# Performance work log

Hardware: AMD Instinct MI355X
Metric: run time of the kernel (lower is better)

## Reference

```python
import jax, jax.numpy as jnp
import numpy as np

THRESH = 0.1

def _ternary_ste(w):
    # STE: forward = ternary(w), backward = identity
    wq = jnp.where(w > THRESH, 1.0, jnp.where(w < -THRESH, -1.0, 0.0))
    return w + jax.lax.stop_gradient(wq - w)

def _act_quant_ste(x):
    # training-mode ActivationQuantizer: scale = 127/max|x| (buffer update, detached)
    scale = jax.lax.stop_gradient(127.0 / jnp.max(jnp.abs(x)))
    xq = jnp.clip(jnp.round(x * scale), -128.0, 127.0) / scale
    return x + jax.lax.stop_gradient(xq - x)

def setup_inputs() -> dict:
    key = jax.random.key(0)
    k1, k2, k3, k4, k5 = jax.random.split(key, 5)
    B, D_IN, D_H, D_OUT = 8192, 784, 4096, 10
    x = jax.random.normal(k1, (B, D_IN), dtype=jnp.float32)
    w1 = jax.random.normal(k2, (D_H, D_IN), dtype=jnp.float32) * 0.05
    b1 = jax.random.normal(k3, (D_H,), dtype=jnp.float32) * 0.01
    w2 = jax.random.normal(k4, (D_OUT, D_H), dtype=jnp.float32) * 0.05
    b2 = jax.random.normal(k5, (D_OUT,), dtype=jnp.float32) * 0.01
    return {"x": x, "w1": w1, "b1": b1, "w2": w2, "b2": b2}

def reference(x, w1, b1, w2, b2):
    x = x.reshape(-1, 784)
    h = x @ _ternary_ste(w1).T + b1          # [B, D_H]
    h = jax.nn.relu(h)
    h = _act_quant_ste(h)
    logits = h @ _ternary_ste(w2).T + b2     # [B, D_OUT]
    return jax.nn.log_softmax(logits, axis=1)
```

## Files before the change

kernel.cpp:

```cpp
#include <hip/hip_runtime.h>

#define M_B   8192
#define K_IN  784
#define KPAD  832
#define N_H   4096
#define N_OUT 10
#define BM    128
#define BN    128
#define BK    64

typedef __attribute__((ext_vector_type(8))) short bf16x8;
typedef __attribute__((ext_vector_type(4))) float f32x4;
typedef unsigned short u16;
typedef unsigned int   u32;

__device__ __forceinline__ u16 f2bf(float f) {
    union { float f; u32 u; } v; v.f = f;
    u32 r = (v.u + 0x7fffu + ((v.u >> 16) & 1u)) >> 16;
    return (u16)r;
}
__device__ __forceinline__ void load_lds16(const void* g, void* l) {
    __builtin_amdgcn_global_load_lds(
        (const __attribute__((address_space(1))) void*)g,
        (__attribute__((address_space(3))) void*)l, 16, 0, 0);
}

__global__ void prep_all(const float* __restrict__ x, const float* __restrict__ w1,
                         const float* __restrict__ w2,
                         u16* __restrict__ xb, u16* __restrict__ w1b,
                         signed char* __restrict__ w2c, float* __restrict__ plog) {
    const int blk = blockIdx.x;
    const int tid = threadIdx.x;
    if (blk < 3328) {
        int idx = blk * 256 + tid;
        int row = idx / 104;
        int col = (idx - row * 104) * 8;
        u16 v[8];
        if (col < K_IN) {
            const float4* p = (const float4*)(x + (size_t)row * K_IN + col);
            float4 a = p[0], b = p[1];
            v[0] = f2bf(a.x); v[1] = f2bf(a.y); v[2] = f2bf(a.z); v[3] = f2bf(a.w);
            v[4] = f2bf(b.x); v[5] = f2bf(b.y); v[6] = f2bf(b.z); v[7] = f2bf(b.w);
        } else {
            #pragma unroll
            for (int i = 0; i < 8; ++i) v[i] = 0;
        }
        *(uint4*)(xb + (size_t)row * KPAD + col) = *(const uint4*)v;
    } else if (blk < 4992) {
        int idx = (blk - 3328) * 256 + tid;
        int row = idx / 104;
        int col = (idx - row * 104) * 8;
        u16 v[8];
        if (col < K_IN) {
            const float4* p = (const float4*)(w1 + (size_t)row * K_IN + col);
            float4 a = p[0], b = p[1];
            float ff[8] = {a.x, a.y, a.z, a.w, b.x, b.y, b.z, b.w};
            #pragma unroll
            for (int i = 0; i < 8; ++i)
                v[i] = ff[i] > 0.1f ? 0x3F80u : (ff[i] < -0.1f ? 0xBF80u : 0u);
        } else {
            #pragma unroll
            for (int i = 0; i < 8; ++i) v[i] = 0;
        }
        *(uint4*)(w1b + (size_t)row * KPAD + col) = *(const uint4*)v;
    } else if (blk < 5008) {
        int k = (blk - 4992) * 256 + tid;
        if (k >= N_H) return;
        signed char v[16];
        #pragma unroll
        for (int o = 0; o < 16; ++o) v[o] = 0;
        #pragma unroll
        for (int o = 0; o < N_OUT; ++o) {
            float f = w2[(size_t)o * N_H + k];
            v[o] = f > 0.1f ? 1 : (f < -0.1f ? -1 : 0);
        }
        *(int4*)(w2c + (size_t)k * 16) = *(const int4*)v;
    } else {
        int idx = (blk - 5008) * 256 + tid;
        ((uint4*)plog)[idx] = make_uint4(0, 0, 0, 0);
    }
}

__global__ __launch_bounds__(256, 3) void gemm_fused(
    const u16* __restrict__ Wb,
    const u16* __restrict__ Xb,
    const float* __restrict__ b1,
    const signed char* __restrict__ W2c,
    float* __restrict__ plog)
{
    __shared__ __align__(16) u16 As[BM * BK];
    __shared__ __align__(16) u16 Bs[BN * BK];
    __shared__ __align__(16) signed char sW2[128 * 16];
    __shared__ float sB1[128];

    const int tid  = threadIdx.x;
    const int lane = tid & 63;
    const int wave = tid >> 6;
    const int wr = wave >> 1, wc = wave & 1;
    const int bm = blockIdx.x;
    const int bn = blockIdx.y;

    if (tid < 128) {
        *(int4*)&sW2[tid * 16] = *(const int4*)(W2c + (size_t)(bm * 128 + tid) * 16);
        sB1[tid] = b1[bm * 128 + tid];
    }

    f32x4 acc[4][4] = {};

    const u16* ga[4]; u16* la[4];
    #pragma unroll
    for (int j = 0; j < 4; ++j) {
        int s = tid + 256 * j;
        int grow = s >> 3;
        int gcol = (((s & 7) ^ ((s >> 3) & 7)) << 3);
        ga[j] = Wb + (size_t)(bm * BM + grow) * KPAD + gcol;
        la[j] = &As[s * 8];
    }
    const u16* gb[4]; u16* lb[4];
    #pragma unroll
    for (int j = 0; j < 4; ++j) {
        int s = tid + 256 * j;
        int grow = s >> 3;
        int gcol = (((s & 7) ^ ((s >> 3) & 7)) << 3);
        gb[j] = Xb + (size_t)(bn * BN + grow) * KPAD + gcol;
        lb[j] = &Bs[s * 8];
    }

    const int rA = (wr * 64 + (lane & 15)) * BK;
    const int rB = (wc * 64 + (lane & 15)) * BK;
    const int c0 = (((lane >> 4) ^ (lane & 7)) << 3);

    for (int t = 0; t < 13; ++t) {
        #pragma unroll
        for (int j = 0; j < 4; ++j) { load_lds16(ga[j], la[j]); ga[j] += BK; }
        #pragma unroll
        for (int j = 0; j < 4; ++j) { load_lds16(gb[j], lb[j]); gb[j] += BK; }
        __syncthreads();

        #pragma unroll
        for (int h = 0; h < 2; ++h) {
            const int ch = c0 ^ (h << 5);
            bf16x8 af[4], bfr[4];
            #pragma unroll
            for (int i = 0; i < 4; ++i) af[i]  = *(const bf16x8*)&As[rA + i * 16 * BK + ch];
            #pragma unroll
            for (int j = 0; j < 4; ++j) bfr[j] = *(const bf16x8*)&Bs[rB + j * 16 * BK + ch];
            #pragma unroll
            for (int i = 0; i < 4; ++i)
                #pragma unroll
                for (int j = 0; j < 4; ++j)
                    acc[i][j] = __builtin_amdgcn_mfma_f32_16x16x32_bf16(
                        af[i], bfr[j], acc[i][j], 0, 0, 0);
        }
        __syncthreads();
    }

    const int quad = lane >> 4;
    const int o = lane & 15;

    bf16x8 wf[4];
    #pragma unroll
    for (int i = 0; i < 4; ++i) {
        #pragma unroll
        for (int jj = 0; jj < 4; ++jj) {
            signed char s8 = sW2[(wr * 64 + i * 16 + quad * 4 + jj) * 16 + o];
            wf[i][jj] = (s8 == 0) ? (short)0 : (s8 > 0 ? (short)0x3F80 : (short)0xBF80);
            wf[i][jj + 4] = 0;
        }
    }
    float4 bias[4];
    #pragma unroll
    for (int i = 0; i < 4; ++i)
        bias[i] = *(const float4*)&sB1[wr * 64 + i * 16 + quad * 4];

    f32x4 d2[4] = {};
    #pragma unroll
    for (int jb = 0; jb < 4; ++jb) {
        #pragma unroll
        for (int i = 0; i < 4; ++i) {
            bf16x8 hf;
            const float* bi = (const float*)&bias[i];
            #pragma unroll
            for (int r = 0; r < 4; ++r) {
                float v = fmaxf(acc[i][jb][r] + bi[r], 0.f);
                hf[r] = (short)f2bf(v);
                hf[r + 4] = 0;
            }
            d2[jb] = __builtin_amdgcn_mfma_f32_16x16x32_bf16(hf, wf[i], d2[jb], 0, 0, 0);
        }
    }

    if (o < N_OUT) {
        #pragma unroll
        for (int jb = 0; jb < 4; ++jb) {
            const int bbase = bn * BN + wc * 64 + jb * 16 + quad * 4;
            #pragma unroll
            for (int r = 0; r < 4; ++r)
                atomicAdd(&plog[(size_t)(bbase + r) * 16 + o], d2[jb][r]);
        }
    }
}

__global__ __launch_bounds__(128) void lsm_out(
    const float* __restrict__ plog,
    const float* __restrict__ b2,
    float* __restrict__ out)
{
    const int b = blockIdx.x * 128 + threadIdx.x;

    float4 p0 = *(const float4*)(plog + (size_t)b * 16);
    float4 p1 = *(const float4*)(plog + (size_t)b * 16 + 4);
    float4 p2 = *(const float4*)(plog + (size_t)b * 16 + 8);
    float p[10] = {p0.x, p0.y, p0.z, p0.w, p1.x, p1.y, p1.z, p1.w, p2.x, p2.y};

    float lg[N_OUT], mx = -1e30f;
    #pragma unroll
    for (int o = 0; o < N_OUT; ++o) {
        lg[o] = p[o] + b2[o];
        mx = fmaxf(mx, lg[o]);
    }
    float se = 0.f;
    #pragma unroll
    for (int o = 0; o < N_OUT; ++o) se += expf(lg[o] - mx);
    const float lse = logf(se) + mx;
    float* op = out + (size_t)b * N_OUT;
    #pragma unroll
    for (int o = 0; o < N_OUT; ++o) op[o] = lg[o] - lse;
}

extern "C" void kernel_launch(void* const* d_in, const int* in_sizes, int n_in,
                              void* d_out, int out_size, void* d_ws, size_t ws_size,
                              hipStream_t stream) {
    const float* x  = (const float*)d_in[0];
    const float* w1 = (const float*)d_in[1];
    const float* b1 = (const float*)d_in[2];
    const float* w2 = (const float*)d_in[3];
    const float* b2 = (const float*)d_in[4];
    float* out = (float*)d_out;

    char* ws = (char*)d_ws;
    u16* xb  = (u16*)(ws);
    u16* w1b = (u16*)(ws + 13631488);
    signed char* w2c = (signed char*)(ws + 20447232);
    float* plog = (float*)(ws + 20512768);

    prep_all<<<5136, 256, 0, stream>>>(x, w1, w2, xb, w1b, w2c, plog);
    gemm_fused<<<dim3(32, 64), 256, 0, stream>>>(w1b, xb, b1, w2c, plog);
    lsm_out<<<64, 128, 0, stream>>>(plog, b2, out);
}
```

Before: 144.2 us.

## Rewrite fused GEMM as 256x256 tile with double-buffered LDS pipeline

Replaces the 128x128 single-buffered GEMM tile with a 256x256 tile computed by 8 waves, using a 128 KB double-buffered LDS layout. Global-to-LDS loads for later k-tiles are issued while MFMAs run on the current buffer, with manual vmcnt/lgkmcnt waits, barriers, sched_barrier and setprio. It also remaps block indices for L2 locality and reads W2/b1 directly from global memory in the epilogue. The larger tile cuts redundant global loads, but it raises register pressure (128 accumulator floats per thread), limits occupancy, and adds many barriers.

```diff
diff --git a/kernel.cpp b/kernel.cpp
--- a/kernel.cpp
+++ b/kernel.cpp
@@ -5,9 +5,7 @@
 #define KPAD  832
 #define N_H   4096
 #define N_OUT 10
-#define BM    128
-#define BN    128
-#define BK    64
+#define TILES 13
 
 typedef __attribute__((ext_vector_type(8))) short bf16x8;
 typedef __attribute__((ext_vector_type(4))) float f32x4;
@@ -81,119 +79,156 @@
     }
 }
 
-__global__ __launch_bounds__(256, 3) void gemm_fused(
+
+#define BAR()    asm volatile("s_barrier" ::: "memory")
+#define LGKM0()  asm volatile("s_waitcnt lgkmcnt(0)" ::: "memory")
+#define VM6()    asm volatile("s_waitcnt vmcnt(6)" ::: "memory")
+#define VM0()    asm volatile("s_waitcnt vmcnt(0)" ::: "memory")
+#define SCHED0() __builtin_amdgcn_sched_barrier(0)
+
+__global__ __launch_bounds__(512, 2) void gemm_fused(
     const u16* __restrict__ Wb,
     const u16* __restrict__ Xb,
     const float* __restrict__ b1,
     const signed char* __restrict__ W2c,
     float* __restrict__ plog)
 {
-    __shared__ __align__(16) u16 As[BM * BK];
-    __shared__ __align__(16) u16 Bs[BN * BK];
-    __shared__ __align__(16) signed char sW2[128 * 16];
-    __shared__ float sB1[128];
+    __shared__ __align__(128) u16 lds[65536];
 
     const int tid  = threadIdx.x;
     const int lane = tid & 63;
     const int wave = tid >> 6;
-    const int wr = wave >> 1, wc = wave & 1;
-    const int bm = blockIdx.x;
-    const int bn = blockIdx.y;
-
-    if (tid < 128) {
-        *(int4*)&sW2[tid * 16] = *(const int4*)(W2c + (size_t)(bm * 128 + tid) * 16);
-        sB1[tid] = b1[bm * 128 + tid];
-    }
-
-    f32x4 acc[4][4] = {};
-
-    const u16* ga[4]; u16* la[4];
-    #pragma unroll
-    for (int j = 0; j < 4; ++j) {
-        int s = tid + 256 * j;
-        int grow = s >> 3;
-        int gcol = (((s & 7) ^ ((s >> 3) & 7)) << 3);
-        ga[j] = Wb + (size_t)(bm * BM + grow) * KPAD + gcol;
-        la[j] = &As[s * 8];
-    }
-    const u16* gb[4]; u16* lb[4];
-    #pragma unroll
-    for (int j = 0; j < 4; ++j) {
-        int s = tid + 256 * j;
-        int grow = s >> 3;
-        int gcol = (((s & 7) ^ ((s >> 3) & 7)) << 3);
-        gb[j] = Xb + (size_t)(bn * BN + grow) * KPAD + gcol;
-        lb[j] = &Bs[s * 8];
-    }
-
-    const int rA = (wr * 64 + (lane & 15)) * BK;
-    const int rB = (wc * 64 + (lane & 15)) * BK;
-    const int c0 = (((lane >> 4) ^ (lane & 7)) << 3);
-
-    for (int t = 0; t < 13; ++t) {
-        #pragma unroll
-        for (int j = 0; j < 4; ++j) { load_lds16(ga[j], la[j]); ga[j] += BK; }
-        #pragma unroll
-        for (int j = 0; j < 4; ++j) { load_lds16(gb[j], lb[j]); gb[j] += BK; }
-        __syncthreads();
-
-        #pragma unroll
-        for (int h = 0; h < 2; ++h) {
-            const int ch = c0 ^ (h << 5);
-            bf16x8 af[4], bfr[4];
-            #pragma unroll
-            for (int i = 0; i < 4; ++i) af[i]  = *(const bf16x8*)&As[rA + i * 16 * BK + ch];
-            #pragma unroll
-            for (int j = 0; j < 4; ++j) bfr[j] = *(const bf16x8*)&Bs[rB + j * 16 * BK + ch];
-            #pragma unroll
-            for (int i = 0; i < 4; ++i)
-                #pragma unroll
-                for (int j = 0; j < 4; ++j)
-                    acc[i][j] = __builtin_amdgcn_mfma_f32_16x16x32_bf16(
-                        af[i], bfr[j], acc[i][j], 0, 0, 0);
-        }
-        __syncthreads();
-    }
+    const int wr = wave >> 2;
+    const int wc = wave & 3;
+
+    const int bid = blockIdx.x;
+    const int swz = (bid & 7) * 64 + (bid >> 3);
+    const int bm = swz & 15;
+    const int bn = swz >> 4;
+
+    const int srow = tid >> 2;
+    const int co   = (tid & 3) ^ ((srow >> 1) & 3);
+    const u16* gA0 = Wb + (size_t)(bm * 256 + srow) * KPAD + co * 8;
+    const u16* gA1 = gA0 + (size_t)128 * KPAD;
+    const u16* gB0 = Xb + (size_t)(bn * 256 + srow) * KPAD + co * 8;
+    const u16* gB1 = gB0 + (size_t)128 * KPAD;
+
+    const int lm    = lane & 15;
+    const int aLane = lm * 32 + ((((lane >> 4) ^ (lm >> 1)) & 3) << 3);
+    const int aBase = wr * 4096 + aLane;
+    const int bBase = 32768 + wc * 2048 + aLane;
+
+    f32x4 acc[8][4] = {};
+    bf16x8 bfr[4];
+
+#define STAGE(SOP, SP0, SP1, ST, SKH)                                      \
+    if ((ST) < TILES) {                                                    \
+      const int rb = (SOP)*32768 + ((ST)&1)*16384 + (SKH)*8192 + tid*8;    \
+      load_lds16(SP0 + (ST)*64 + (SKH)*32, lds + rb);                      \
+      load_lds16(SP1 + (ST)*64 + (SKH)*32, lds + rb + 4096);               \
+    }
+
+#define RD_A(BUF, KH, IH)                                                  \
+    { const u16* pa = lds + aBase + ((BUF)*16384 + (KH)*8192 + (IH)*2048); \
+      af[0] = *(const bf16x8*)(pa);                                        \
+      af[1] = *(const bf16x8*)(pa + 512);                                  \
+      af[2] = *(const bf16x8*)(pa + 1024);                                 \
+      af[3] = *(const bf16x8*)(pa + 1536); }
+
+#define RD_B(BUF, KH)                                                      \
+    { const u16* pb = lds + bBase + ((BUF)*16384 + (KH)*8192);             \
+      bfr[0] = *(const bf16x8*)(pb);                                       \
+      bfr[1] = *(const bf16x8*)(pb + 512);                                 \
+      bfr[2] = *(const bf16x8*)(pb + 1024);                                \
+      bfr[3] = *(const bf16x8*)(pb + 1536); }
+
+#define MFMA16(IH)                                                         \
+    __builtin_amdgcn_s_setprio(1);                                         \
+    _Pragma("unroll")                                                      \
+    for (int ii = 0; ii < 4; ++ii)                                         \
+      _Pragma("unroll")                                                    \
+      for (int jb = 0; jb < 4; ++jb)                                       \
+        acc[(IH)*4 + ii][jb] = __builtin_amdgcn_mfma_f32_16x16x32_bf16(    \
+            af[ii], bfr[jb], acc[(IH)*4 + ii][jb], 0, 0, 0);               \
+    __builtin_amdgcn_s_setprio(0);
+
+    STAGE(0, gA0, gA1, 0, 0);
+    STAGE(1, gB0, gB1, 0, 0);
+    STAGE(0, gA0, gA1, 0, 1);
+    STAGE(1, gB0, gB1, 0, 1);
+    STAGE(1, gB0, gB1, 1, 0);
+    STAGE(0, gA0, gA1, 1, 0);
+    STAGE(1, gB0, gB1, 1, 1);
+    VM6(); BAR();
+
+    #pragma unroll 1
+    for (int i = 0; i < 6; ++i) {
+        const int t1 = 2 * i + 1, t2 = 2 * i + 2, t3 = 2 * i + 3;
+        { bf16x8 af[4]; RD_A(0,0,0); RD_B(0,0); STAGE(0, gA0, gA1, t1, 1);
+          BAR(); LGKM0(); SCHED0(); MFMA16(0); } BAR();
+        { bf16x8 af[4]; RD_A(0,0,1);            STAGE(1, gB0, gB1, t2, 0);
+          BAR(); LGKM0(); SCHED0(); MFMA16(1); } BAR();
+        { bf16x8 af[4]; RD_A(0,1,0); RD_B(0,1); STAGE(0, gA0, gA1, t2, 0);
+          BAR(); LGKM0(); SCHED0(); MFMA16(0); } BAR();
+        { bf16x8 af[4]; RD_A(0,1,1);            STAGE(1, gB0, gB1, t2, 1);
+          BAR(); LGKM0(); SCHED0(); MFMA16(1); } VM6(); BAR();
+        { bf16x8 af[4]; RD_A(1,0,0); RD_B(1,0); STAGE(0, gA0, gA1, t2, 1);
+          BAR(); LGKM0(); SCHED0(); MFMA16(0); } BAR();
+        { bf16x8 af[4]; RD_A(1,0,1);            STAGE(1, gB0, gB1, t3, 0);
+          BAR(); LGKM0(); SCHED0(); MFMA16(1); } BAR();
+        { bf16x8 af[4]; RD_A(1,1,0); RD_B(1,1); STAGE(0, gA0, gA1, t3, 0);
+          BAR(); LGKM0(); SCHED0(); MFMA16(0); } BAR();
+        { bf16x8 af[4]; RD_A(1,1,1);            STAGE(1, gB0, gB1, t3, 1);
+          BAR(); LGKM0(); SCHED0(); MFMA16(1); } VM6(); BAR();
+    }
+
+    VM0(); BAR();
+    { bf16x8 af[4]; RD_A(0,0,0); RD_B(0,0); MFMA16(0); }
+    { bf16x8 af[4]; RD_A(0,0,1);            MFMA16(1); }
+    { bf16x8 af[4]; RD_A(0,1,0); RD_B(0,1); MFMA16(0); }
+    { bf16x8 af[4]; RD_A(0,1,1);            MFMA16(1); }
 
     const int quad = lane >> 4;
-    const int o = lane & 15;
-
-    bf16x8 wf[4];
-    #pragma unroll
-    for (int i = 0; i < 4; ++i) {
+    const int o = lm;
+    const int jrow = bm * 256 + wr * 128 + quad * 4;
+
+    bf16x8 wf[8];
+    #pragma unroll
+    for (int ii = 0; ii < 8; ++ii) {
         #pragma unroll
         for (int jj = 0; jj < 4; ++jj) {
-            signed char s8 = sW2[(wr * 64 + i * 16 + quad * 4 + jj) * 16 + o];
-            wf[i][jj] = (s8 == 0) ? (short)0 : (s8 > 0 ? (short)0x3F80 : (short)0xBF80);
-            wf[i][jj + 4] = 0;
-        }
-    }
-    float4 bias[4];
-    #pragma unroll
-    for (int i = 0; i < 4; ++i)
-        bias[i] = *(const float4*)&sB1[wr * 64 + i * 16 + quad * 4];
+            signed char s8 = W2c[(size_t)(jrow + ii * 16 + jj) * 16 + o];
+            wf[ii][jj] = (s8 == 0) ? (short)0
+                                   : (s8 > 0 ? (short)0x3F80 : (short)0xBF80);
+            wf[ii][jj + 4] = 0;
+        }
+    }
+    float4 bias[8];
+    #pragma unroll
+    for (int ii = 0; ii < 8; ++ii)
+        bias[ii] = *(const float4*)(b1 + jrow + ii * 16);
 
     f32x4 d2[4] = {};
     #pragma unroll
     for (int jb = 0; jb < 4; ++jb) {
         #pragma unroll
-        for (int i = 0; i < 4; ++i) {
+        for (int ii = 0; ii < 8; ++ii) {
             bf16x8 hf;
-            const float* bi = (const float*)&bias[i];
+            const float* bi = (const float*)&bias[ii];
             #pragma unroll
             for (int r = 0; r < 4; ++r) {
-                float v = fmaxf(acc[i][jb][r] + bi[r], 0.f);
+                float v = fmaxf(acc[ii][jb][r] + bi[r], 0.f);
                 hf[r] = (short)f2bf(v);
                 hf[r + 4] = 0;
             }
-            d2[jb] = __builtin_amdgcn_mfma_f32_16x16x32_bf16(hf, wf[i], d2[jb], 0, 0, 0);
+            d2[jb] = __builtin_amdgcn_mfma_f32_16x16x32_bf16(hf, wf[ii], d2[jb], 0, 0, 0);
         }
     }
 
     if (o < N_OUT) {
         #pragma unroll
         for (int jb = 0; jb < 4; ++jb) {
-            const int bbase = bn * BN + wc * 64 + jb * 16 + quad * 4;
+            const int bbase = bn * 256 + wc * 64 + jb * 16 + quad * 4;
             #pragma unroll
             for (int r = 0; r < 4; ++r)
                 atomicAdd(&plog[(size_t)(bbase + r) * 16 + o], d2[jb][r]);
@@ -245,6 +280,6 @@
     float* plog = (float*)(ws + 20512768);
 
     prep_all<<<5136, 256, 0, stream>>>(x, w1, w2, xb, w1b, w2c, plog);
-    gemm_fused<<<dim3(32, 64), 256, 0, stream>>>(w1b, xb, b1, w2c, plog);
+    gemm_fused<<<512, 512, 0, stream>>>(w1b, xb, b1, w2c, plog);
     lsm_out<<<64, 128, 0, stream>>>(plog, b2, out);
 }
```

Result: no change. 145.4 us (+0.9%).

## Fuse log-softmax into GEMM via last-block counter and widen prep per-thread work

Applied to the files above, without the earlier changes.

Removes the separate log-softmax kernel launch. Each GEMM block bumps a per-row-tile atomic counter, and the last of the 32 contributing blocks computes log-softmax for its 128 rows. The prep kernel now converts 16 elements per thread instead of 8, halving the number of blocks. In exchange, every GEMM block adds a threadfence and an atomic, and the tail work is serialised onto the last-arriving block.

```diff
diff --git a/kernel.cpp b/kernel.cpp
--- a/kernel.cpp
+++ b/kernel.cpp
@@ -28,43 +28,51 @@
 __global__ void prep_all(const float* __restrict__ x, const float* __restrict__ w1,
                          const float* __restrict__ w2,
                          u16* __restrict__ xb, u16* __restrict__ w1b,
-                         signed char* __restrict__ w2c, float* __restrict__ plog) {
+                         signed char* __restrict__ w2c, float* __restrict__ plog,
+                         int* __restrict__ cnt) {
     const int blk = blockIdx.x;
     const int tid = threadIdx.x;
-    if (blk < 3328) {
+    if (blk < 1664) {
         int idx = blk * 256 + tid;
-        int row = idx / 104;
-        int col = (idx - row * 104) * 8;
-        u16 v[8];
+        int row = idx / 52;
+        int col = (idx - row * 52) * 16;
+        u16 v[16];
         if (col < K_IN) {
             const float4* p = (const float4*)(x + (size_t)row * K_IN + col);
-            float4 a = p[0], b = p[1];
-            v[0] = f2bf(a.x); v[1] = f2bf(a.y); v[2] = f2bf(a.z); v[3] = f2bf(a.w);
-            v[4] = f2bf(b.x); v[5] = f2bf(b.y); v[6] = f2bf(b.z); v[7] = f2bf(b.w);
+            float4 a = p[0], b = p[1], c = p[2], d = p[3];
+            float ff[16] = {a.x,a.y,a.z,a.w, b.x,b.y,b.z,b.w,
+                            c.x,c.y,c.z,c.w, d.x,d.y,d.z,d.w};
+            #pragma unroll
+            for (int i = 0; i < 16; ++i) v[i] = f2bf(ff[i]);
         } else {
             #pragma unroll
-            for (int i = 0; i < 8; ++i) v[i] = 0;
-        }
-        *(uint4*)(xb + (size_t)row * KPAD + col) = *(const uint4*)v;
-    } else if (blk < 4992) {
-        int idx = (blk - 3328) * 256 + tid;
-        int row = idx / 104;
-        int col = (idx - row * 104) * 8;
-        u16 v[8];
+            for (int i = 0; i < 16; ++i) v[i] = 0;
+        }
+        u16* dst = xb + (size_t)row * KPAD + col;
+        *(uint4*)(dst)     = *(const uint4*)(v);
+        *(uint4*)(dst + 8) = *(const uint4*)(v + 8);
+    } else if (blk < 2496) {
+        int idx = (blk - 1664) * 256 + tid;
+        int row = idx / 52;
+        int col = (idx - row * 52) * 16;
+        u16 v[16];
         if (col < K_IN) {
             const float4* p = (const float4*)(w1 + (size_t)row * K_IN + col);
-            float4 a = p[0], b = p[1];
-            float ff[8] = {a.x, a.y, a.z, a.w, b.x, b.y, b.z, b.w};
-            #pragma unroll
-            for (int i = 0; i < 8; ++i)
+            float4 a = p[0], b = p[1], c = p[2], d = p[3];
+            float ff[16] = {a.x,a.y,a.z,a.w, b.x,b.y,b.z,b.w,
+                            c.x,c.y,c.z,c.w, d.x,d.y,d.z,d.w};
+            #pragma unroll
+            for (int i = 0; i < 16; ++i)
                 v[i] = ff[i] > 0.1f ? 0x3F80u : (ff[i] < -0.1f ? 0xBF80u : 0u);
         } else {
             #pragma unroll
-            for (int i = 0; i < 8; ++i) v[i] = 0;
-        }
-        *(uint4*)(w1b + (size_t)row * KPAD + col) = *(const uint4*)v;
-    } else if (blk < 5008) {
-        int k = (blk - 4992) * 256 + tid;
+            for (int i = 0; i < 16; ++i) v[i] = 0;
+        }
+        u16* dst = w1b + (size_t)row * KPAD + col;
+        *(uint4*)(dst)     = *(const uint4*)(v);
+        *(uint4*)(dst + 8) = *(const uint4*)(v + 8);
+    } else if (blk < 2512) {
+        int k = (blk - 2496) * 256 + tid;
         if (k >= N_H) return;
         signed char v[16];
         #pragma unroll
@@ -76,8 +84,9 @@
         }
         *(int4*)(w2c + (size_t)k * 16) = *(const int4*)v;
     } else {
-        int idx = (blk - 5008) * 256 + tid;
+        int idx = (blk - 2512) * 256 + tid;
         ((uint4*)plog)[idx] = make_uint4(0, 0, 0, 0);
+        if (idx < 16) ((uint4*)cnt)[idx] = make_uint4(0, 0, 0, 0);
     }
 }
 
@@ -86,12 +95,16 @@
     const u16* __restrict__ Xb,
     const float* __restrict__ b1,
     const signed char* __restrict__ W2c,
-    float* __restrict__ plog)
+    float* __restrict__ plog,
+    const float* __restrict__ b2,
+    float* __restrict__ out,
+    int* __restrict__ cnt)
 {
     __shared__ __align__(16) u16 As[BM * BK];
     __shared__ __align__(16) u16 Bs[BN * BK];
     __shared__ __align__(16) signed char sW2[128 * 16];
     __shared__ float sB1[128];
+    __shared__ int sLast;
 
     const int tid  = threadIdx.x;
     const int lane = tid & 63;
@@ -199,33 +212,33 @@
                 atomicAdd(&plog[(size_t)(bbase + r) * 16 + o], d2[jb][r]);
         }
     }
-}
-
-__global__ __launch_bounds__(128) void lsm_out(
-    const float* __restrict__ plog,
-    const float* __restrict__ b2,
-    float* __restrict__ out)
-{
-    const int b = blockIdx.x * 128 + threadIdx.x;
-
-    float4 p0 = *(const float4*)(plog + (size_t)b * 16);
-    float4 p1 = *(const float4*)(plog + (size_t)b * 16 + 4);
-    float4 p2 = *(const float4*)(plog + (size_t)b * 16 + 8);
-    float p[10] = {p0.x, p0.y, p0.z, p0.w, p1.x, p1.y, p1.z, p1.w, p2.x, p2.y};
-
-    float lg[N_OUT], mx = -1e30f;
-    #pragma unroll
-    for (int o = 0; o < N_OUT; ++o) {
-        lg[o] = p[o] + b2[o];
-        mx = fmaxf(mx, lg[o]);
-    }
-    float se = 0.f;
-    #pragma unroll
-    for (int o = 0; o < N_OUT; ++o) se += expf(lg[o] - mx);
-    const float lse = logf(se) + mx;
-    float* op = out + (size_t)b * N_OUT;
-    #pragma unroll
-    for (int o = 0; o < N_OUT; ++o) op[o] = lg[o] - lse;
+
+    __threadfence();
+    if (tid == 0) {
+        int old = __hip_atomic_fetch_add(&cnt[bn], 1, __ATOMIC_ACQ_REL,
+                                         __HIP_MEMORY_SCOPE_AGENT);
+        sLast = (old == 31);
+    }
+    __syncthreads();
+    if (sLast && tid < 128) {
+        __threadfence();
+        const int row = bn * BN + tid;
+        float lg[N_OUT], mx = -1e30f;
+        #pragma unroll
+        for (int oo = 0; oo < N_OUT; ++oo) {
+            float pv = __hip_atomic_load(&plog[(size_t)row * 16 + oo],
+                                         __ATOMIC_RELAXED, __HIP_MEMORY_SCOPE_AGENT);
+            lg[oo] = pv + b2[oo];
+            mx = fmaxf(mx, lg[oo]);
+        }
+        float se = 0.f;
+        #pragma unroll
+        for (int oo = 0; oo < N_OUT; ++oo) se += expf(lg[oo] - mx);
+        const float lse = logf(se) + mx;
+        float* op = out + (size_t)row * N_OUT;
+        #pragma unroll
+        for (int oo = 0; oo < N_OUT; ++oo) op[oo] = lg[oo] - lse;
+    }
 }
 
 extern "C" void kernel_launch(void* const* d_in, const int* in_sizes, int n_in,
@@ -243,8 +256,8 @@
     u16* w1b = (u16*)(ws + 13631488);
     signed char* w2c = (signed char*)(ws + 20447232);
     float* plog = (float*)(ws + 20512768);
-
-    prep_all<<<5136, 256, 0, stream>>>(x, w1, w2, xb, w1b, w2c, plog);
-    gemm_fused<<<dim3(32, 64), 256, 0, stream>>>(w1b, xb, b1, w2c, plog);
-    lsm_out<<<64, 128, 0, stream>>>(plog, b2, out);
-}
+    int* cnt = (int*)(ws + 21037056);
+
+    prep_all<<<2640, 256, 0, stream>>>(x, w1, w2, xb, w1b, w2c, plog, cnt);
+    gemm_fused<<<dim3(32, 64), 256, 0, stream>>>(w1b, xb, b1, w2c, plog, b2, out, cnt);
+}
```

Result: slower. 381.3 us (+164.5%).
